# Optimization experiments

Measured on AMD Instinct MI355X. Metric: run time of the kernel, lower is better.

The kernel has to match this reference:

```python
import jax, jax.numpy as jnp
import numpy as np

B = 65536
IN_DIM, H1, H2, TGT = 768, 512, 384, 256
N_SUB, K = 16, 256
SUB_DIM = TGT // N_SUB  # 16


def setup_inputs() -> dict:
    key = jax.random.key(0)
    ks = jax.random.split(key, 8)
    sc = lambda fan_in: 1.0 / np.sqrt(fan_in)
    return {
        "x": jax.random.normal(ks[0], (B, IN_DIM), dtype=jnp.float32),
        "W1": jax.random.uniform(ks[1], (IN_DIM, H1), jnp.float32, -sc(IN_DIM), sc(IN_DIM)),
        "b1": jnp.zeros((H1,), jnp.float32),
        "W2": jax.random.uniform(ks[2], (H1, H2), jnp.float32, -sc(H1), sc(H1)),
        "b2": jnp.zeros((H2,), jnp.float32),
        "W3": jax.random.uniform(ks[3], (H2, TGT), jnp.float32, -sc(H2), sc(H2)),
        "b3": jnp.zeros((TGT,), jnp.float32),
        "codebooks": jax.random.normal(ks[4], (N_SUB, K, SUB_DIM), jnp.float32) * 0.1,
    }


def reference(x, W1, b1, W2, b2, W3, b3, codebooks):
    # Encoder MLP (GELU exact, dropout inactive at eval)
    h = jax.nn.gelu(x @ W1 + b1, approximate=False)
    h = jax.nn.gelu(h @ W2 + b2, approximate=False)
    encoded = h @ W3 + b3                      # [B, TGT]

    e = encoded.reshape(-1, N_SUB, SUB_DIM)    # [B, S, d]
    # squared distances ||e - c||^2 = ||e||^2 - 2 e.c + ||c||^2 -> [B, S, K]
    e2 = jnp.sum(e * e, axis=-1)[:, :, None]
    c2 = jnp.sum(codebooks * codebooks, axis=-1)[None, :, :]
    ec = jnp.einsum("bsd,skd->bsk", e, codebooks)
    distances = e2 - 2.0 * ec + c2
    codes = jnp.argmin(distances, axis=-1)     # [B, S]
    # gather: quantized[b, s] = codebooks[s, codes[b, s]]
    quantized = codebooks[jnp.arange(N_SUB)[None, :], codes]  # [B, S, d]
    return quantized.reshape(-1, TGT)
```

## Files before the change

### kernel.cpp

```cpp
#include <hip/hip_runtime.h>
#include <hip/hip_bf16.h>
#include <math.h>


#define IN_DIM 768
#define HD1    512
#define HD2    384
#define TGT    256
#define NSUB   16
#define KCODE  256
#define SUBD   16
#define RPB    8
#define NT     256

__device__ __forceinline__ double gelu64(double v) {
    return 0.5 * v * (1.0 + erf(v * 0.70710678118654752440084436210485));
}

__global__ __launch_bounds__(NT) void fused_mlp_pq_f64(
    const float* __restrict__ x,
    const float* __restrict__ W1, const float* __restrict__ b1,
    const float* __restrict__ W2, const float* __restrict__ b2,
    const float* __restrict__ W3, const float* __restrict__ b3,
    const float* __restrict__ cbs,
    float* __restrict__ out)
{
    __shared__ double lds[RPB * HD1 + RPB * HD2];
    double* h1s  = lds;
    double* h2s  = lds + RPB * HD1;
    double* encs = lds;

    const int t = threadIdx.x;
    const size_t row0 = (size_t)blockIdx.x * RPB;

    {
        const int rg = t >> 7, cg = t & 127;
        const int c0 = cg << 2;
        const int r0 = rg << 2;
        double acc[4][4];
        #pragma unroll
        for (int j = 0; j < 4; ++j)
            #pragma unroll
            for (int c = 0; c < 4; ++c) acc[j][c] = 0.0;

        const float* xr0 = x + (row0 + r0) * IN_DIM;
        const float* xr1 = xr0 + IN_DIM;
        const float* xr2 = xr1 + IN_DIM;
        const float* xr3 = xr2 + IN_DIM;
        const float* wp  = W1 + c0;

        for (int k = 0; k < IN_DIM; k += 4) {
            float4 a0 = *(const float4*)(xr0 + k);
            float4 a1 = *(const float4*)(xr1 + k);
            float4 a2 = *(const float4*)(xr2 + k);
            float4 a3 = *(const float4*)(xr3 + k);
            #pragma unroll
            for (int kk = 0; kk < 4; ++kk) {
                float4 w = *(const float4*)(wp);
                wp += HD1;
                double w0 = (double)w.x, w1 = (double)w.y;
                double w2 = (double)w.z, w3 = (double)w.w;
                double av0 = (double)((const float*)&a0)[kk];
                double av1 = (double)((const float*)&a1)[kk];
                double av2 = (double)((const float*)&a2)[kk];
                double av3 = (double)((const float*)&a3)[kk];
                acc[0][0] = fma(av0, w0, acc[0][0]); acc[0][1] = fma(av0, w1, acc[0][1]);
                acc[0][2] = fma(av0, w2, acc[0][2]); acc[0][3] = fma(av0, w3, acc[0][3]);
                acc[1][0] = fma(av1, w0, acc[1][0]); acc[1][1] = fma(av1, w1, acc[1][1]);
                acc[1][2] = fma(av1, w2, acc[1][2]); acc[1][3] = fma(av1, w3, acc[1][3]);
                acc[2][0] = fma(av2, w0, acc[2][0]); acc[2][1] = fma(av2, w1, acc[2][1]);
                acc[2][2] = fma(av2, w2, acc[2][2]); acc[2][3] = fma(av2, w3, acc[2][3]);
                acc[3][0] = fma(av3, w0, acc[3][0]); acc[3][1] = fma(av3, w1, acc[3][1]);
                acc[3][2] = fma(av3, w2, acc[3][2]); acc[3][3] = fma(av3, w3, acc[3][3]);
            }
        }
        double bb[4];
        #pragma unroll
        for (int c = 0; c < 4; ++c) bb[c] = (double)b1[c0 + c];
        #pragma unroll
        for (int j = 0; j < 4; ++j)
            #pragma unroll
            for (int c = 0; c < 4; ++c)
                h1s[(r0 + j) * HD1 + c0 + c] = gelu64(acc[j][c] + bb[c]);
    }
    __syncthreads();

    {
        const int rg = t >> 7, cg = t & 127;
        const int c0 = cg * 3;
        const int r0 = rg << 2;
        double acc[4][3];
        #pragma unroll
        for (int j = 0; j < 4; ++j)
            #pragma unroll
            for (int c = 0; c < 3; ++c) acc[j][c] = 0.0;

        const double* hr0 = h1s + r0 * HD1;
        const double* hr1 = hr0 + HD1;
        const double* hr2 = hr1 + HD1;
        const double* hr3 = hr2 + HD1;
        const float* wp = W2 + c0;

        for (int k = 0; k < HD1; k += 2) {
            double2 a0 = *(const double2*)(hr0 + k);
            double2 a1 = *(const double2*)(hr1 + k);
            double2 a2 = *(const double2*)(hr2 + k);
            double2 a3 = *(const double2*)(hr3 + k);
            #pragma unroll
            for (int kk = 0; kk < 2; ++kk) {
                double w0 = (double)wp[0];
                double w1 = (double)wp[1];
                double w2 = (double)wp[2];
                wp += HD2;
                double av0 = kk ? a0.y : a0.x;
                double av1 = kk ? a1.y : a1.x;
                double av2 = kk ? a2.y : a2.x;
                double av3 = kk ? a3.y : a3.x;
                acc[0][0] = fma(av0, w0, acc[0][0]); acc[0][1] = fma(av0, w1, acc[0][1]); acc[0][2] = fma(av0, w2, acc[0][2]);
                acc[1][0] = fma(av1, w0, acc[1][0]); acc[1][1] = fma(av1, w1, acc[1][1]); acc[1][2] = fma(av1, w2, acc[1][2]);
                acc[2][0] = fma(av2, w0, acc[2][0]); acc[2][1] = fma(av2, w1, acc[2][1]); acc[2][2] = fma(av2, w2, acc[2][2]);
                acc[3][0] = fma(av3, w0, acc[3][0]); acc[3][1] = fma(av3, w1, acc[3][1]); acc[3][2] = fma(av3, w2, acc[3][2]);
            }
        }
        double bb[3];
        #pragma unroll
        for (int c = 0; c < 3; ++c) bb[c] = (double)b2[c0 + c];
        #pragma unroll
        for (int j = 0; j < 4; ++j)
            #pragma unroll
            for (int c = 0; c < 3; ++c)
                h2s[(r0 + j) * HD2 + c0 + c] = gelu64(acc[j][c] + bb[c]);
    }
    __syncthreads();

    {
        const int rg = t >> 7, cg = t & 127;
        const int c0 = cg << 1;
        const int r0 = rg << 2;
        double acc[4][2];
        #pragma unroll
        for (int j = 0; j < 4; ++j)
            #pragma unroll
            for (int c = 0; c < 2; ++c) acc[j][c] = 0.0;

        const double* hr0 = h2s + r0 * HD2;
        const double* hr1 = hr0 + HD2;
        const double* hr2 = hr1 + HD2;
        const double* hr3 = hr2 + HD2;
        const float* wp = W3 + c0;

        for (int k = 0; k < HD2; k += 2) {
            double2 a0 = *(const double2*)(hr0 + k);
            double2 a1 = *(const double2*)(hr1 + k);
            double2 a2 = *(const double2*)(hr2 + k);
            double2 a3 = *(const double2*)(hr3 + k);
            #pragma unroll
            for (int kk = 0; kk < 2; ++kk) {
                double w0 = (double)wp[0];
                double w1 = (double)wp[1];
                wp += TGT;
                double av0 = kk ? a0.y : a0.x;
                double av1 = kk ? a1.y : a1.x;
                double av2 = kk ? a2.y : a2.x;
                double av3 = kk ? a3.y : a3.x;
                acc[0][0] = fma(av0, w0, acc[0][0]); acc[0][1] = fma(av0, w1, acc[0][1]);
                acc[1][0] = fma(av1, w0, acc[1][0]); acc[1][1] = fma(av1, w1, acc[1][1]);
                acc[2][0] = fma(av2, w0, acc[2][0]); acc[2][1] = fma(av2, w1, acc[2][1]);
                acc[3][0] = fma(av3, w0, acc[3][0]); acc[3][1] = fma(av3, w1, acc[3][1]);
            }
        }
        double bb[2];
        #pragma unroll
        for (int c = 0; c < 2; ++c) bb[c] = (double)b3[c0 + c];
        #pragma unroll
        for (int j = 0; j < 4; ++j)
            #pragma unroll
            for (int c = 0; c < 2; ++c)
                encs[(r0 + j) * TGT + c0 + c] = acc[j][c] + bb[c];
    }
    __syncthreads();

    {
        const int r = t >> 5;
        const int s = (t >> 1) & 15;
        const int half = t & 1;

        double e[16];
        const double* ep = encs + r * TGT + s * SUBD;
        #pragma unroll
        for (int d = 0; d < 16; ++d) e[d] = ep[d];

        const float* cbS = cbs + (size_t)s * KCODE * SUBD;
        const float* cbH = cbS + half * 128 * SUBD;

        double best = 1.0e300;
        int bi = 0;
        for (int kk = 0; kk < 128; ++kk) {
            const float4* cp = (const float4*)(cbH + kk * SUBD);
            float4 c0 = cp[0], c1 = cp[1], c2 = cp[2], c3 = cp[3];
            double dist = 0.0;
            double dd;
            dd = (double)c0.x - e[0];  dist = fma(dd, dd, dist);
            dd = (double)c0.y - e[1];  dist = fma(dd, dd, dist);
            dd = (double)c0.z - e[2];  dist = fma(dd, dd, dist);
            dd = (double)c0.w - e[3];  dist = fma(dd, dd, dist);
            dd = (double)c1.x - e[4];  dist = fma(dd, dd, dist);
            dd = (double)c1.y - e[5];  dist = fma(dd, dd, dist);
            dd = (double)c1.z - e[6];  dist = fma(dd, dd, dist);
            dd = (double)c1.w - e[7];  dist = fma(dd, dd, dist);
            dd = (double)c2.x - e[8];  dist = fma(dd, dd, dist);
            dd = (double)c2.y - e[9];  dist = fma(dd, dd, dist);
            dd = (double)c2.z - e[10]; dist = fma(dd, dd, dist);
            dd = (double)c2.w - e[11]; dist = fma(dd, dd, dist);
            dd = (double)c3.x - e[12]; dist = fma(dd, dd, dist);
            dd = (double)c3.y - e[13]; dist = fma(dd, dd, dist);
            dd = (double)c3.z - e[14]; dist = fma(dd, dd, dist);
            dd = (double)c3.w - e[15]; dist = fma(dd, dd, dist);
            if (dist < best) { best = dist; bi = kk; }
        }
        bi += half * 128;

        double obest = __shfl_xor(best, 1);
        int    obi   = __shfl_xor(bi, 1);
        if (obest < best || (obest == best && obi < bi)) { best = obest; bi = obi; }

        const float4* sp = (const float4*)(cbS + bi * SUBD);
        float* op = out + (row0 + r) * TGT + s * SUBD;
        if (half == 0) {
            ((float4*)op)[0] = sp[0];
            ((float4*)op)[1] = sp[1];
        } else {
            ((float4*)op)[2] = sp[2];
            ((float4*)op)[3] = sp[3];
        }
    }
}

extern "C" void kernel_launch(void* const* d_in, const int* in_sizes, int n_in,
                              void* d_out, int out_size, void* d_ws, size_t ws_size,
                              hipStream_t stream) {
    const float* x   = (const float*)d_in[0];
    const float* W1  = (const float*)d_in[1];
    const float* b1  = (const float*)d_in[2];
    const float* W2  = (const float*)d_in[3];
    const float* b2  = (const float*)d_in[4];
    const float* W3  = (const float*)d_in[5];
    const float* b3  = (const float*)d_in[6];
    const float* cbs = (const float*)d_in[7];
    float* out = (float*)d_out;

    const int B = in_sizes[0] / IN_DIM;
    dim3 grid(B / RPB), block(NT);
    hipLaunchKernelGGL(fused_mlp_pq_f64, grid, block, 0, stream,
                       x, W1, b1, W2, b2, W3, b3, cbs, out);
}
```

Measured before the change: 4.708 ms.

## Run MLP and PQ search in fp32 with fp64 fixup for near-tie rows

```diff
diff --git a/kernel.cpp b/kernel.cpp
--- a/kernel.cpp
+++ b/kernel.cpp
@@ -10,173 +10,134 @@
 #define NSUB   16
 #define KCODE  256
 #define SUBD   16
-#define RPB    8
-#define NT     256
-
+#define RPB    16
+#define NT_A   512
+#define NT_B   256
+#define TAU    4e-3f
+
+#define FMA4(ACC, S, W)            \
+    ACC.x = fmaf(S, W.x, ACC.x);   \
+    ACC.y = fmaf(S, W.y, ACC.y);   \
+    ACC.z = fmaf(S, W.z, ACC.z);   \
+    ACC.w = fmaf(S, W.w, ACC.w);
+
+__device__ __forceinline__ float gelu32(float v) {
+    return 0.5f * v * (1.0f + erff(v * 0.70710678118654752440f));
+}
 __device__ __forceinline__ double gelu64(double v) {
     return 0.5 * v * (1.0 + erf(v * 0.70710678118654752440084436210485));
 }
 
-__global__ __launch_bounds__(NT) void fused_mlp_pq_f64(
+__global__ __launch_bounds__(NT_A) void mlp_pq_f32(
     const float* __restrict__ x,
     const float* __restrict__ W1, const float* __restrict__ b1,
     const float* __restrict__ W2, const float* __restrict__ b2,
     const float* __restrict__ W3, const float* __restrict__ b3,
     const float* __restrict__ cbs,
-    float* __restrict__ out)
+    float* __restrict__ out,
+    unsigned* __restrict__ cnt, unsigned* __restrict__ wl, unsigned cap)
 {
-    __shared__ double lds[RPB * HD1 + RPB * HD2];
-    double* h1s  = lds;
-    double* h2s  = lds + RPB * HD1;
-    double* encs = lds;
-
-    const int t = threadIdx.x;
+    __shared__ float lds[RPB * HD1 + RPB * HD2];
+    float* h1s  = lds;
+    float* h2s  = lds + RPB * HD1;
+    float* encs = lds;
+
+    const int t  = threadIdx.x;
+    const int rg = t >> 5;
+    const int cg = t & 31;
     const size_t row0 = (size_t)blockIdx.x * RPB;
 
     {
-        const int rg = t >> 7, cg = t & 127;
-        const int c0 = cg << 2;
-        const int r0 = rg << 2;
-        double acc[4][4];
-        #pragma unroll
-        for (int j = 0; j < 4; ++j)
-            #pragma unroll
-            for (int c = 0; c < 4; ++c) acc[j][c] = 0.0;
-
-        const float* xr0 = x + (row0 + r0) * IN_DIM;
-        const float* xr1 = xr0 + IN_DIM;
-        const float* xr2 = xr1 + IN_DIM;
-        const float* xr3 = xr2 + IN_DIM;
-        const float* wp  = W1 + c0;
-
+        float4 acc[4];
+        #pragma unroll
+        for (int q = 0; q < 4; ++q) acc[q] = make_float4(0.f, 0.f, 0.f, 0.f);
+        const int c0 = cg << 4;
+        const float* xr = x + (row0 + rg) * IN_DIM;
+        const float* wp = W1 + c0;
         for (int k = 0; k < IN_DIM; k += 4) {
-            float4 a0 = *(const float4*)(xr0 + k);
-            float4 a1 = *(const float4*)(xr1 + k);
-            float4 a2 = *(const float4*)(xr2 + k);
-            float4 a3 = *(const float4*)(xr3 + k);
-            #pragma unroll
-            for (int kk = 0; kk < 4; ++kk) {
-                float4 w = *(const float4*)(wp);
+            float4 a = *(const float4*)(xr + k);
+            #pragma unroll
+            for (int j = 0; j < 4; ++j) {
+                float4 w0 = *(const float4*)(wp);
+                float4 w1 = *(const float4*)(wp + 4);
+                float4 w2 = *(const float4*)(wp + 8);
+                float4 w3 = *(const float4*)(wp + 12);
+                float s = ((const float*)&a)[j];
+                FMA4(acc[0], s, w0) FMA4(acc[1], s, w1)
+                FMA4(acc[2], s, w2) FMA4(acc[3], s, w3)
                 wp += HD1;
-                double w0 = (double)w.x, w1 = (double)w.y;
-                double w2 = (double)w.z, w3 = (double)w.w;
-                double av0 = (double)((const float*)&a0)[kk];
-                double av1 = (double)((const float*)&a1)[kk];
-                double av2 = (double)((const float*)&a2)[kk];
-                double av3 = (double)((const float*)&a3)[kk];
-                acc[0][0] = fma(av0, w0, acc[0][0]); acc[0][1] = fma(av0, w1, acc[0][1]);
-                acc[0][2] = fma(av0, w2, acc[0][2]); acc[0][3] = fma(av0, w3, acc[0][3]);
-                acc[1][0] = fma(av1, w0, acc[1][0]); acc[1][1] = fma(av1, w1, acc[1][1]);
-                acc[1][2] = fma(av1, w2, acc[1][2]); acc[1][3] = fma(av1, w3, acc[1][3]);
-                acc[2][0] = fma(av2, w0, acc[2][0]); acc[2][1] = fma(av2, w1, acc[2][1]);
-                acc[2][2] = fma(av2, w2, acc[2][2]); acc[2][3] = fma(av2, w3, acc[2][3]);
-                acc[3][0] = fma(av3, w0, acc[3][0]); acc[3][1] = fma(av3, w1, acc[3][1]);
-                acc[3][2] = fma(av3, w2, acc[3][2]); acc[3][3] = fma(av3, w3, acc[3][3]);
-            }
-        }
-        double bb[4];
-        #pragma unroll
-        for (int c = 0; c < 4; ++c) bb[c] = (double)b1[c0 + c];
-        #pragma unroll
-        for (int j = 0; j < 4; ++j)
-            #pragma unroll
-            for (int c = 0; c < 4; ++c)
-                h1s[(r0 + j) * HD1 + c0 + c] = gelu64(acc[j][c] + bb[c]);
+            }
+        }
+        #pragma unroll
+        for (int q = 0; q < 4; ++q) {
+            float4 bb = *(const float4*)(b1 + c0 + (q << 2));
+            float4 g;
+            g.x = gelu32(acc[q].x + bb.x);
+            g.y = gelu32(acc[q].y + bb.y);
+            g.z = gelu32(acc[q].z + bb.z);
+            g.w = gelu32(acc[q].w + bb.w);
+            *(float4*)&h1s[rg * HD1 + c0 + (q << 2)] = g;
+        }
     }
     __syncthreads();
 
     {
-        const int rg = t >> 7, cg = t & 127;
-        const int c0 = cg * 3;
-        const int r0 = rg << 2;
-        double acc[4][3];
-        #pragma unroll
-        for (int j = 0; j < 4; ++j)
-            #pragma unroll
-            for (int c = 0; c < 3; ++c) acc[j][c] = 0.0;
-
-        const double* hr0 = h1s + r0 * HD1;
-        const double* hr1 = hr0 + HD1;
-        const double* hr2 = hr1 + HD1;
-        const double* hr3 = hr2 + HD1;
+        float4 acc[3];
+        #pragma unroll
+        for (int q = 0; q < 3; ++q) acc[q] = make_float4(0.f, 0.f, 0.f, 0.f);
+        const int c0 = cg * 12;
+        const float* hr = h1s + rg * HD1;
         const float* wp = W2 + c0;
-
-        for (int k = 0; k < HD1; k += 2) {
-            double2 a0 = *(const double2*)(hr0 + k);
-            double2 a1 = *(const double2*)(hr1 + k);
-            double2 a2 = *(const double2*)(hr2 + k);
-            double2 a3 = *(const double2*)(hr3 + k);
-            #pragma unroll
-            for (int kk = 0; kk < 2; ++kk) {
-                double w0 = (double)wp[0];
-                double w1 = (double)wp[1];
-                double w2 = (double)wp[2];
+        for (int k = 0; k < HD1; k += 4) {
+            float4 a = *(const float4*)(hr + k);
+            #pragma unroll
+            for (int j = 0; j < 4; ++j) {
+                float4 w0 = *(const float4*)(wp);
+                float4 w1 = *(const float4*)(wp + 4);
+                float4 w2 = *(const float4*)(wp + 8);
+                float s = ((const float*)&a)[j];
+                FMA4(acc[0], s, w0) FMA4(acc[1], s, w1) FMA4(acc[2], s, w2)
                 wp += HD2;
-                double av0 = kk ? a0.y : a0.x;
-                double av1 = kk ? a1.y : a1.x;
-                double av2 = kk ? a2.y : a2.x;
-                double av3 = kk ? a3.y : a3.x;
-                acc[0][0] = fma(av0, w0, acc[0][0]); acc[0][1] = fma(av0, w1, acc[0][1]); acc[0][2] = fma(av0, w2, acc[0][2]);
-                acc[1][0] = fma(av1, w0, acc[1][0]); acc[1][1] = fma(av1, w1, acc[1][1]); acc[1][2] = fma(av1, w2, acc[1][2]);
-                acc[2][0] = fma(av2, w0, acc[2][0]); acc[2][1] = fma(av2, w1, acc[2][1]); acc[2][2] = fma(av2, w2, acc[2][2]);
-                acc[3][0] = fma(av3, w0, acc[3][0]); acc[3][1] = fma(av3, w1, acc[3][1]); acc[3][2] = fma(av3, w2, acc[3][2]);
-            }
-        }
-        double bb[3];
-        #pragma unroll
-        for (int c = 0; c < 3; ++c) bb[c] = (double)b2[c0 + c];
-        #pragma unroll
-        for (int j = 0; j < 4; ++j)
-            #pragma unroll
-            for (int c = 0; c < 3; ++c)
-                h2s[(r0 + j) * HD2 + c0 + c] = gelu64(acc[j][c] + bb[c]);
+            }
+        }
+        #pragma unroll
+        for (int q = 0; q < 3; ++q) {
+            float4 bb = *(const float4*)(b2 + c0 + (q << 2));
+            float4 g;
+            g.x = gelu32(acc[q].x + bb.x);
+            g.y = gelu32(acc[q].y + bb.y);
+            g.z = gelu32(acc[q].z + bb.z);
+            g.w = gelu32(acc[q].w + bb.w);
+            *(float4*)&h2s[rg * HD2 + c0 + (q << 2)] = g;
+        }
     }
     __syncthreads();
 
     {
-        const int rg = t >> 7, cg = t & 127;
-        const int c0 = cg << 1;
-        const int r0 = rg << 2;
-        double acc[4][2];
-        #pragma unroll
-        for (int j = 0; j < 4; ++j)
-            #pragma unroll
-            for (int c = 0; c < 2; ++c) acc[j][c] = 0.0;
-
-        const double* hr0 = h2s + r0 * HD2;
-        const double* hr1 = hr0 + HD2;
-        const double* hr2 = hr1 + HD2;
-        const double* hr3 = hr2 + HD2;
+        float4 acc[2];
+        #pragma unroll
+        for (int q = 0; q < 2; ++q) acc[q] = make_float4(0.f, 0.f, 0.f, 0.f);
+        const int c0 = cg << 3;
+        const float* hr = h2s + rg * HD2;
         const float* wp = W3 + c0;
-
-        for (int k = 0; k < HD2; k += 2) {
-            double2 a0 = *(const double2*)(hr0 + k);
-            double2 a1 = *(const double2*)(hr1 + k);
-            double2 a2 = *(const double2*)(hr2 + k);
-            double2 a3 = *(const double2*)(hr3 + k);
-            #pragma unroll
-            for (int kk = 0; kk < 2; ++kk) {
-                double w0 = (double)wp[0];
-                double w1 = (double)wp[1];
+        for (int k = 0; k < HD2; k += 4) {
+            float4 a = *(const float4*)(hr + k);
+            #pragma unroll
+            for (int j = 0; j < 4; ++j) {
+                float4 w0 = *(const float4*)(wp);
+                float4 w1 = *(const float4*)(wp + 4);
+                float s = ((const float*)&a)[j];
+                FMA4(acc[0], s, w0) FMA4(acc[1], s, w1)
                 wp += TGT;
-                double av0 = kk ? a0.y : a0.x;
-                double av1 = kk ? a1.y : a1.x;
-                double av2 = kk ? a2.y : a2.x;
-                double av3 = kk ? a3.y : a3.x;
-                acc[0][0] = fma(av0, w0, acc[0][0]); acc[0][1] = fma(av0, w1, acc[0][1]);
-                acc[1][0] = fma(av1, w0, acc[1][0]); acc[1][1] = fma(av1, w1, acc[1][1]);
-                acc[2][0] = fma(av2, w0, acc[2][0]); acc[2][1] = fma(av2, w1, acc[2][1]);
-                acc[3][0] = fma(av3, w0, acc[3][0]); acc[3][1] = fma(av3, w1, acc[3][1]);
-            }
-        }
-        double bb[2];
-        #pragma unroll
-        for (int c = 0; c < 2; ++c) bb[c] = (double)b3[c0 + c];
-        #pragma unroll
-        for (int j = 0; j < 4; ++j)
-            #pragma unroll
-            for (int c = 0; c < 2; ++c)
-                encs[(r0 + j) * TGT + c0 + c] = acc[j][c] + bb[c];
+            }
+        }
+        #pragma unroll
+        for (int q = 0; q < 2; ++q) {
+            float4 bb = *(const float4*)(b3 + c0 + (q << 2));
+            float4 e = acc[q];
+            e.x += bb.x; e.y += bb.y; e.z += bb.z; e.w += bb.w;
+            *(float4*)&encs[rg * TGT + c0 + (q << 2)] = e;
+        }
     }
     __syncthreads();
 
@@ -185,46 +146,48 @@
         const int s = (t >> 1) & 15;
         const int half = t & 1;
 
-        double e[16];
-        const double* ep = encs + r * TGT + s * SUBD;
-        #pragma unroll
-        for (int d = 0; d < 16; ++d) e[d] = ep[d];
+        float tv[16];
+        const float* ep = encs + r * TGT + s * SUBD;
+        #pragma unroll
+        for (int d = 0; d < 16; ++d) tv[d] = -2.0f * ep[d];
 
         const float* cbS = cbs + (size_t)s * KCODE * SUBD;
         const float* cbH = cbS + half * 128 * SUBD;
 
-        double best = 1.0e300;
-        int bi = 0;
+        float l1 = 3.402823466e38f, l2 = 3.402823466e38f;
+        int li = 0;
         for (int kk = 0; kk < 128; ++kk) {
             const float4* cp = (const float4*)(cbH + kk * SUBD);
             float4 c0 = cp[0], c1 = cp[1], c2 = cp[2], c3 = cp[3];
-            double dist = 0.0;
-            double dd;
-            dd = (double)c0.x - e[0];  dist = fma(dd, dd, dist);
-            dd = (double)c0.y - e[1];  dist = fma(dd, dd, dist);
-            dd = (double)c0.z - e[2];  dist = fma(dd, dd, dist);
-            dd = (double)c0.w - e[3];  dist = fma(dd, dd, dist);
-            dd = (double)c1.x - e[4];  dist = fma(dd, dd, dist);
-            dd = (double)c1.y - e[5];  dist = fma(dd, dd, dist);
-            dd = (double)c1.z - e[6];  dist = fma(dd, dd, dist);
-            dd = (double)c1.w - e[7];  dist = fma(dd, dd, dist);
-            dd = (double)c2.x - e[8];  dist = fma(dd, dd, dist);
-            dd = (double)c2.y - e[9];  dist = fma(dd, dd, dist);
-            dd = (double)c2.z - e[10]; dist = fma(dd, dd, dist);
-            dd = (double)c2.w - e[11]; dist = fma(dd, dd, dist);
-            dd = (double)c3.x - e[12]; dist = fma(dd, dd, dist);
-            dd = (double)c3.y - e[13]; dist = fma(dd, dd, dist);
-            dd = (double)c3.z - e[14]; dist = fma(dd, dd, dist);
-            dd = (double)c3.w - e[15]; dist = fma(dd, dd, dist);
-            if (dist < best) { best = dist; bi = kk; }
-        }
-        bi += half * 128;
-
-        double obest = __shfl_xor(best, 1);
-        int    obi   = __shfl_xor(bi, 1);
-        if (obest < best || (obest == best && obi < bi)) { best = obest; bi = obi; }
-
-        const float4* sp = (const float4*)(cbS + bi * SUBD);
+            float d0 = c0.x*(c0.x+tv[0]) + c0.y*(c0.y+tv[1]) + c0.z*(c0.z+tv[2]) + c0.w*(c0.w+tv[3]);
+            float d1 = c1.x*(c1.x+tv[4]) + c1.y*(c1.y+tv[5]) + c1.z*(c1.z+tv[6]) + c1.w*(c1.w+tv[7]);
+            float d2 = c2.x*(c2.x+tv[8]) + c2.y*(c2.y+tv[9]) + c2.z*(c2.z+tv[10]) + c2.w*(c2.w+tv[11]);
+            float d3 = c3.x*(c3.x+tv[12]) + c3.y*(c3.y+tv[13]) + c3.z*(c3.z+tv[14]) + c3.w*(c3.w+tv[15]);
+            float dist = (d0 + d1) + (d2 + d3);
+            if (dist < l1)      { l2 = l1; l1 = dist; li = kk; }
+            else if (dist < l2) { l2 = dist; }
+        }
+        int idx = li + half * 128;
+
+        float o1 = __shfl_xor(l1, 1);
+        float o2 = __shfl_xor(l2, 1);
+        int   oi = __shfl_xor(idx, 1);
+        float g1, g2; int gi;
+        if (o1 < l1)      { g1 = o1; gi = oi; g2 = fminf(l1, o2); }
+        else if (o1 > l1) { g1 = l1; gi = idx; g2 = fminf(o1, l2); }
+        else              { g1 = l1; gi = (oi < idx) ? oi : idx; g2 = l1; }
+
+        bool flagged = (g2 - g1) < TAU;
+        unsigned long long mask = __ballot(flagged);
+        if ((t & 31) == 0) {
+            unsigned rm = (unsigned)(mask >> (t & 32));
+            if (rm) {
+                unsigned p = atomicAdd(cnt, 1u);
+                if (p < cap) wl[p] = (unsigned)(row0 + r);
+            }
+        }
+
+        const float4* sp = (const float4*)(cbS + gi * SUBD);
         float* op = out + (row0 + r) * TGT + s * SUBD;
         if (half == 0) {
             ((float4*)op)[0] = sp[0];
@@ -232,6 +195,115 @@
         } else {
             ((float4*)op)[2] = sp[2];
             ((float4*)op)[3] = sp[3];
+        }
+    }
+}
+
+__global__ __launch_bounds__(NT_B) void fixup_f64(
+    const float* __restrict__ x,
+    const float* __restrict__ W1, const float* __restrict__ b1,
+    const float* __restrict__ W2, const float* __restrict__ b2,
+    const float* __restrict__ W3, const float* __restrict__ b3,
+    const float* __restrict__ cbs,
+    float* __restrict__ out,
+    const unsigned* __restrict__ cnt, const unsigned* __restrict__ wl,
+    unsigned cap)
+{
+    __shared__ double xr[IN_DIM];
+    __shared__ double h1[HD1];
+    __shared__ double h2[HD2];
+    __shared__ double en[TGT];
+
+    const int t = threadIdx.x;
+    unsigned n = *cnt;
+    if (n > cap) n = cap;
+
+    for (unsigned w = blockIdx.x; w < n; w += gridDim.x) {
+        const size_t row = wl[w];
+        __syncthreads();
+
+        const float* xp = x + row * IN_DIM;
+        xr[t]       = (double)xp[t];
+        xr[t + 256] = (double)xp[t + 256];
+        xr[t + 512] = (double)xp[t + 512];
+        __syncthreads();
+
+        {
+            double a0 = 0.0, a1 = 0.0;
+            for (int k = 0; k < IN_DIM; ++k) {
+                double xv = xr[k];
+                a0 = fma(xv, (double)W1[k * HD1 + t], a0);
+                a1 = fma(xv, (double)W1[k * HD1 + t + 256], a1);
+            }
+            h1[t]       = gelu64(a0 + (double)b1[t]);
+            h1[t + 256] = gelu64(a1 + (double)b1[t + 256]);
+        }
+        __syncthreads();
+
+        if (t < 192) {
+            double a0 = 0.0, a1 = 0.0;
+            for (int k = 0; k < HD1; ++k) {
+                double hv = h1[k];
+                a0 = fma(hv, (double)W2[k * HD2 + t], a0);
+                a1 = fma(hv, (double)W2[k * HD2 + t + 192], a1);
+            }
+            h2[t]       = gelu64(a0 + (double)b2[t]);
+            h2[t + 192] = gelu64(a1 + (double)b2[t + 192]);
+        }
+        __syncthreads();
+
+        {
+            double a0 = 0.0;
+            for (int k = 0; k < HD2; ++k)
+                a0 = fma(h2[k], (double)W3[k * TGT + t], a0);
+            en[t] = a0 + (double)b3[t];
+        }
+        __syncthreads();
+
+        {
+            const int s = t >> 4;
+            const int c16 = t & 15;
+            double e[16];
+            #pragma unroll
+            for (int d = 0; d < 16; ++d) e[d] = en[s * SUBD + d];
+
+            const float* cbS = cbs + (size_t)s * KCODE * SUBD;
+            const float* cbL = cbS + (c16 * 16) * SUBD;
+
+            double best = 1.0e300;
+            int bi = c16 * 16;
+            for (int kk = 0; kk < 16; ++kk) {
+                const float4* cp = (const float4*)(cbL + kk * SUBD);
+                float4 c0 = cp[0], c1 = cp[1], c2 = cp[2], c3 = cp[3];
+                double dist = 0.0, dd;
+                dd = (double)c0.x - e[0];  dist = fma(dd, dd, dist);
+                dd = (double)c0.y - e[1];  dist = fma(dd, dd, dist);
+                dd = (double)c0.z - e[2];  dist = fma(dd, dd, dist);
+                dd = (double)c0.w - e[3];  dist = fma(dd, dd, dist);
+                dd = (double)c1.x - e[4];  dist = fma(dd, dd, dist);
+                dd = (double)c1.y - e[5];  dist = fma(dd, dd, dist);
+                dd = (double)c1.z - e[6];  dist = fma(dd, dd, dist);
+                dd = (double)c1.w - e[7];  dist = fma(dd, dd, dist);
+                dd = (double)c2.x - e[8];  dist = fma(dd, dd, dist);
+                dd = (double)c2.y - e[9];  dist = fma(dd, dd, dist);
+                dd = (double)c2.z - e[10]; dist = fma(dd, dd, dist);
+                dd = (double)c2.w - e[11]; dist = fma(dd, dd, dist);
+                dd = (double)c3.x - e[12]; dist = fma(dd, dd, dist);
+                dd = (double)c3.y - e[13]; dist = fma(dd, dd, dist);
+                dd = (double)c3.z - e[14]; dist = fma(dd, dd, dist);
+                dd = (double)c3.w - e[15]; dist = fma(dd, dd, dist);
+                if (dist < best) { best = dist; bi = c16 * 16 + kk; }
+            }
+            #pragma unroll
+            for (int off = 1; off < 16; off <<= 1) {
+                double od = __shfl_xor(best, off);
+                int    oi = __shfl_xor(bi, off);
+                if (od < best || (od == best && oi < bi)) { best = od; bi = oi; }
+            }
+            if (c16 < 4) {
+                float4 v = ((const float4*)(cbS + bi * SUBD))[c16];
+                ((float4*)(out + row * TGT + s * SUBD))[c16] = v;
+            }
         }
     }
 }
@@ -250,7 +322,14 @@
     float* out = (float*)d_out;
 
     const int B = in_sizes[0] / IN_DIM;
-    dim3 grid(B / RPB), block(NT);
-    hipLaunchKernelGGL(fused_mlp_pq_f64, grid, block, 0, stream,
-                       x, W1, b1, W2, b2, W3, b3, cbs, out);
-}
+    unsigned* cnt = (unsigned*)d_ws;
+    unsigned* wl  = cnt + 1;
+    size_t cap_sz = (ws_size / sizeof(unsigned)) - 1;
+    unsigned cap = (unsigned)(cap_sz > 65536 ? 65536 : cap_sz);
+
+    hipMemsetAsync(d_ws, 0, sizeof(unsigned), stream);
+    hipLaunchKernelGGL(mlp_pq_f32, dim3(B / RPB), dim3(NT_A), 0, stream,
+                       x, W1, b1, W2, b2, W3, b3, cbs, out, cnt, wl, cap);
+    hipLaunchKernelGGL(fixup_f64, dim3(2048), dim3(NT_B), 0, stream,
+                       x, W1, b1, W2, b2, W3, b3, cbs, out, cnt, wl, cap);
+}
```

Result: slower. 17.69 ms (+275.7%).
